# Kernel tuning notes

Hardware: AMD Instinct MI355X
Metric: run time of the kernel (lower is better)

Reference implementation:

```python
import jax, jax.numpy as jnp
import numpy as np

MIN_VAL = 1e-10


def integ_exp_trig(lam, theta, t, t0=None):
    # Analytic integrals of exp(lam*s)*cos(theta*s) and exp(lam*s)*sin(theta*s) on [t0, t].
    if t0 is None:
        t0 = jnp.zeros_like(t)
    exps_t = jnp.nan_to_num(jnp.exp(lam * t))
    exps_t0 = jnp.nan_to_num(jnp.exp(lam * t0))
    denom = jnp.square(lam) + jnp.square(theta)
    scale = jnp.sign(denom) / jnp.clip(denom, MIN_VAL)
    cos_t, sin_t = jnp.cos(theta * t), jnp.sin(theta * t)
    cos_t0, sin_t0 = jnp.cos(theta * t0), jnp.sin(theta * t0)
    res_cos = scale * (exps_t * (lam * cos_t + theta * sin_t)
                       - exps_t0 * (lam * cos_t0 + theta * sin_t0))
    res_sin = scale * (exps_t * (lam * sin_t - theta * cos_t)
                       - exps_t0 * (lam * sin_t0 - theta * cos_t0))
    return jnp.nan_to_num(res_cos), jnp.nan_to_num(res_sin)


def esde_predict_complex(X0, X0_var, U, times, Q, lam_real, lam_imag, V_real, V_imag):
    B, n = X0.shape
    m = n // 2
    lam = lam_real + 1j * lam_imag          # [B, m] complex
    V = V_real + 1j * V_imag                # [B, n, m] complex
    X0c = X0[:, :, None]                    # [B, n, 1]

    # Phi(0): exp(0*lam) = 1, so phi_comp = V
    Phi0 = jnp.concatenate([V.real, V.imag], axis=2)        # [B, n, n]
    Phi0_inv = jnp.nan_to_num(jnp.linalg.inv(Phi0))

    init_cond = Phi0_inv @ X0c                               # [B, n, 1]
    init_var = Phi0_inv @ X0_var @ jnp.swapaxes(Phi0_inv, -1, -2)

    # Phi(t)
    et = jnp.exp(times[:, None].astype(lam.dtype) * lam)     # [B, m] complex
    phi = V * et[:, None, :]                                 # right-mult by diag(et)
    Phi = jnp.nan_to_num(jnp.concatenate([phi.real, phi.imag], axis=2))  # [B, n, n]

    Hom = Phi @ init_cond
    Hom_var = Phi @ init_var @ jnp.swapaxes(Phi, -1, -2)
    # force positive diagonal: diag -> |diag|, off-diag unchanged
    eye = jnp.eye(n, dtype=Hom_var.dtype)
    diag_sign = jnp.sign(jnp.diagonal(Hom_var, axis1=-2, axis2=-1))  # [B, n]
    Hom_var = Hom_var * ((1.0 - eye) + eye * diag_sign[:, :, None])

    # ----- particular (control) term: block 2x2 rotation-integral times Phi0_inv @ U
    ext_u = (Phi0_inv @ U[:, :, None]).reshape(B, m, 2)      # interleaved (re, im) pairs
    cos_int, sin_int = integ_exp_trig(-lam.real, lam.imag, times[:, None])  # [B, m]
    li0 = cos_int * ext_u[..., 0] - sin_int * ext_u[..., 1]
    li1 = sin_int * ext_u[..., 0] + cos_int * ext_u[..., 1]
    lambda_int = jnp.stack([li0, li1], axis=-1).reshape(B, n, 1)
    Part = Phi @ lambda_int

    # ----- diffusion variance term
    ext_s = Phi0_inv @ Q @ jnp.swapaxes(Phi0_inv, -1, -2)    # [B, n, n]
    ls = lam[:, None, :] + lam[:, :, None]                   # lam_i + lam_j
    ls_conj = lam[:, None, :] - lam[:, :, None]              # lam_j - lam_i
    t3 = times[:, None, None]
    cos1, sin1 = integ_exp_trig(-ls.real, ls.imag, t3)       # [B, m, m]
    cos2, sin2 = integ_exp_trig(-ls.real, ls_conj.imag, t3)
    vcc = 0.5 * (cos1 + cos2)   # int cos*cos
    vsc = 0.5 * (sin1 + sin2)   # int sin*cos
    vcs = 0.5 * (sin1 - sin2)   # int cos*sin
    vss = 0.5 * (cos2 - cos1)   # int sin*sin
    E = ext_s.reshape(B, m, 2, m, 2)  # interleaved 2x2 block structure
    d11, d12 = E[:, :, 0, :, 0], E[:, :, 0, :, 1]
    d21, d22 = E[:, :, 1, :, 0], E[:, :, 1, :, 1]
    r11 = vcc * d11 - vsc * d21 - vcs * d12 + vss * d22
    r12 = vcs * d11 - vss * d21 + vcc * d12 - vsc * d22
    r21 = vsc * d11 + vcc * d21 - vss * d12 - vcs * d22
    r22 = vss * d11 + vcs * d21 + vsc * d12 + vcc * d22
    row0 = jnp.stack([r11, r12], axis=-1)   # [B, m, m, 2]
    row1 = jnp.stack([r21, r22], axis=-1)
    sig_int = jnp.stack([row0, row1], axis=2).reshape(B, n, n)
    Part_var = Phi @ sig_int @ jnp.swapaxes(Phi, -1, -2)

    return Hom + Part, Hom_var + Part_var


def setup_inputs() -> dict:
    key = jax.random.key(0)
    ks = jax.random.split(key, 9)
    B, n = 65536, 16
    m = n // 2
    X0 = jax.random.normal(ks[0], (B, n), jnp.float32)
    A = jax.random.normal(ks[1], (B, n, n), jnp.float32) * 0.1
    X0_var = A @ jnp.swapaxes(A, -1, -2) + 0.1 * jnp.eye(n, dtype=jnp.float32)
    U = jax.random.normal(ks[2], (B, n), jnp.float32)
    times = jax.random.uniform(ks[3], (B,), jnp.float32, 0.1, 2.0)
    Qa = jax.random.normal(ks[4], (B, n, n), jnp.float32) * 0.1
    Q = Qa @ jnp.swapaxes(Qa, -1, -2)
    lam_real = -jax.random.uniform(ks[5], (B, m), jnp.float32, 0.05, 1.0)
    lam_imag = jax.random.uniform(ks[6], (B, m), jnp.float32, -2.0, 2.0)
    V_real = jax.random.normal(ks[7], (B, n, m), jnp.float32)
    V_imag = jax.random.normal(ks[8], (B, n, m), jnp.float32)
    return {"X0": X0, "X0_var": X0_var, "U": U, "times": times, "Q": Q,
            "lam_real": lam_real, "lam_imag": lam_imag,
            "V_real": V_real, "V_imag": V_imag}


def reference(X0, X0_var, U, times, Q, lam_real, lam_imag, V_real, V_imag):
    return esde_predict_complex(X0, X0_var, U, times, Q,
                                lam_real, lam_imag, V_real, V_imag)
```

## Files before the change

### kernel.cpp

```cpp
#include <hip/hip_runtime.h>
#include <math.h>

#define WSYNC() do { __builtin_amdgcn_wave_barrier(); asm volatile("" ::: "memory"); } while (0)
#define LFENCE() asm volatile("" ::: "memory")

constexpr int FS = 20;

typedef float v2f __attribute__((ext_vector_type(2)));
__device__ inline v2f pkfma(v2f a, v2f b, v2f c) {
  return __builtin_elementwise_fma(a, b, c);
}

struct alignas(16) WaveMem {
  float P[16 * FS];
  float F[16 * FS];
  float W[16 * FS];
  float L4[16 * FS];
  float etr[8], eti[8], lamr[8], lami[8];
  float vx0[16], vu[16], vic[16];
};

__device__ inline float n2n(float v) {
  if (isnan(v)) return 0.0f;
  if (isinf(v)) return v > 0.f ? 3.402823466e38f : -3.402823466e38f;
  return v;
}

__device__ inline float readlane_f(float v, int l) {
  return __int_as_float(__builtin_amdgcn_readlane(__float_as_int(v), l));
}
template<int CTRL>
__device__ inline float dpp_f(float v) {
  return __int_as_float(__builtin_amdgcn_mov_dpp(__float_as_int(v), CTRL, 0xF, 0xF, true));
}

__device__ inline void load16(float out[16], const float* p) {
#pragma unroll
  for (int c = 0; c < 4; ++c) {
    float4 v = *(const float4*)(p + 4 * c);
    out[4*c+0] = v.x; out[4*c+1] = v.y; out[4*c+2] = v.z; out[4*c+3] = v.w;
  }
}

template<bool TRB>
__device__ inline void mmv(float* C, const float* A, const float* Bm,
                           int i16, int jg, bool absdiag = false)
{
  const int j0 = jg << 2;
  float aA[16];
  load16(aA, &A[i16 * FS]);
  float acc[4];
  if (TRB) {
#pragma unroll
    for (int cp = 0; cp < 2; ++cp) {
      float bB0[16], bB1[16];
      load16(bB0, &Bm[(j0 + 2*cp) * FS]);
      load16(bB1, &Bm[(j0 + 2*cp + 1) * FS]);
      v2f s = {0.f, 0.f};
#pragma unroll
      for (int k = 0; k < 16; ++k)
        s = pkfma((v2f){aA[k], aA[k]}, (v2f){bB0[k], bB1[k]}, s);
      acc[2*cp] = s.x; acc[2*cp+1] = s.y;
    }
  } else {
    v2f a01 = {0.f, 0.f}, a23 = {0.f, 0.f};
#pragma unroll
    for (int k = 0; k < 16; ++k) {
      float4 bv = *(const float4*)&Bm[k * FS + j0];
      v2f ad = {aA[k], aA[k]};
      a01 = pkfma(ad, (v2f){bv.x, bv.y}, a01);
      a23 = pkfma(ad, (v2f){bv.z, bv.w}, a23);
    }
    acc[0] = a01.x; acc[1] = a01.y; acc[2] = a23.x; acc[3] = a23.y;
  }
  if (absdiag) {
#pragma unroll
    for (int c = 0; c < 4; ++c) if (i16 == j0 + c) acc[c] = fabsf(acc[c]);
  }
  *(float4*)&C[i16 * FS + j0] = make_float4(acc[0], acc[1], acc[2], acc[3]);
}

__global__ __launch_bounds__(256, 7) void nesde_kernel(
    const float* __restrict__ gX0, const float* __restrict__ gXv,
    const float* __restrict__ gU,  const float* __restrict__ gT,
    const float* __restrict__ gQ,  const float* __restrict__ gLr,
    const float* __restrict__ gLi, const float* __restrict__ gVr,
    const float* __restrict__ gVi, float* __restrict__ gOut0,
    float* __restrict__ gOut1, int B)
{
  __shared__ WaveMem sm[4];
  const int wid  = threadIdx.x >> 6;
  const int lane = threadIdx.x & 63;
  const int b = blockIdx.x * 4 + wid;
  if (b >= B) return;
  WaveMem& S = sm[wid];

  const int r4  = lane >> 2;
  const int q   = lane & 3;
  const int i16 = lane & 15;
  const int jg  = lane >> 4;
  const int j0  = jg << 2;

  const float t = gT[b];

  const float4 xv = *(const float4*)(gXv + (size_t)b * 256 + lane * 4);
  const float4 qv = *(const float4*)(gQ  + (size_t)b * 256 + lane * 4);
  float4 va = make_float4(0.f,0.f,0.f,0.f), vb = va;
  if (q < 2) {
    const float* src = (q == 0) ? gVr : gVi;
    va = *(const float4*)(src + (size_t)b * 128 + r4 * 8);
    vb = *(const float4*)(src + (size_t)b * 128 + r4 * 8 + 4);
  }
  float x0u = 0.f;
  if (q == 2) x0u = gX0[(size_t)b * 16 + r4];
  if (q == 3) x0u = gU [(size_t)b * 16 + r4];

  if (lane < 8) {
    float lr = gLr[(size_t)b * 8 + lane];
    float li = gLi[(size_t)b * 8 + lane];
    S.lamr[lane] = lr; S.lami[lane] = li;
    float e = expf(lr * t);
    float sn, cs; sincosf(li * t, &sn, &cs);
    S.etr[lane] = e * cs;
    S.eti[lane] = e * sn;
  }
  WSYNC();

  float4 vco;
  {
    const int p = lane >> 3, qq = lane & 7;
    float la  = -(S.lamr[p] + S.lamr[qq]);
    float th1 = S.lami[p] + S.lami[qq];
    float th2 = S.lami[qq] - S.lami[p];
    float exps = __expf(la * t);
    float s1, c1, s2, c2;
    __sincosf(th1 * t, &s1, &c1);
    __sincosf(th2 * t, &s2, &c2);
    float den1 = la * la + th1 * th1;
    float sg1 = (den1 > 0.f) ? 1.f : ((den1 < 0.f) ? -1.f : 0.f);
    float sc1 = sg1 / fmaxf(den1, 1e-10f);
    float cos1 = sc1 * (exps * (la * c1 + th1 * s1) - la);
    float sin1 = sc1 * (exps * (la * s1 - th1 * c1) + th1);
    float den2 = la * la + th2 * th2;
    float sg2 = (den2 > 0.f) ? 1.f : ((den2 < 0.f) ? -1.f : 0.f);
    float sc2 = sg2 / fmaxf(den2, 1e-10f);
    float cos2 = sc2 * (exps * (la * c2 + th2 * s2) - la);
    float sin2 = sc2 * (exps * (la * s2 - th2 * c2) + th2);
    vco = make_float4(0.5f * (cos1 + cos2), 0.5f * (sin1 + sin2),
                      0.5f * (sin1 - sin2), 0.5f * (cos2 - cos1));
  }
  {
    const int si = lane >> 2, sj = (lane & 3) * 4;
    *(float4*)&S.L4[si * FS + sj] = qv;
  }
  if (q == 2) S.vx0[r4] = x0u;
  if (q == 3) S.vu[r4]  = x0u;

  float myv[8] = { va.x, va.y, va.z, va.w, vb.x, vb.y, vb.z, vb.w };
  float ov[8];
#pragma unroll
  for (int e = 0; e < 8; ++e) ov[e] = __shfl_xor(myv[e], 1);
  if (q < 2) {
    float er[8], ei[8];
#pragma unroll
    for (int e = 0; e < 8; ++e) { er[e] = S.etr[e]; ei[e] = S.eti[e]; }
    float vr[8], vi[8], ph[8];
#pragma unroll
    for (int e = 0; e < 8; ++e) {
      vr[e] = (q == 0) ? myv[e] : ov[e];
      vi[e] = (q == 0) ? ov[e]  : myv[e];
    }
    if (q == 0) {
#pragma unroll
      for (int e = 0; e < 8; ++e) ph[e] = vr[e] * er[e] - vi[e] * ei[e];
      *(float4*)&S.F[r4 * FS + 0] = make_float4(ph[0], ph[1], ph[2], ph[3]);
      *(float4*)&S.F[r4 * FS + 4] = make_float4(ph[4], ph[5], ph[6], ph[7]);
    } else {
#pragma unroll
      for (int e = 0; e < 8; ++e) ph[e] = vr[e] * ei[e] + vi[e] * er[e];
      *(float4*)&S.F[r4 * FS + 8]  = make_float4(ph[0], ph[1], ph[2], ph[3]);
      *(float4*)&S.F[r4 * FS + 12] = make_float4(ph[4], ph[5], ph[6], ph[7]);
    }
  }

  float a[8];
#pragma unroll
  for (int e = 0; e < 8; ++e) {
    float idv = 0.f;
    if (q == 2) idv = (r4 == e)     ? 1.f : 0.f;
    if (q == 3) idv = (r4 == 8 + e) ? 1.f : 0.f;
    a[e] = (q < 2) ? myv[e] : idv;
  }

  unsigned used = 0;
  int myk = 0;
#pragma unroll
  for (int k = 0; k < 16; ++k) {
    const int qk = k >> 3, ek = k & 7;
    float av = a[ek];
    float ck = (qk == 0) ? dpp_f<0x00>(av) : dpp_f<0x55>(av);
    float cand = ((used >> r4) & 1u) ? -1.0f : fabsf(ck);
    float mx = cand;
    mx = fmaxf(mx, dpp_f<0x124>(mx));
    mx = fmaxf(mx, dpp_f<0x128>(mx));
    mx = fmaxf(mx, dpp_f<0x142>(mx));
    mx = fmaxf(mx, dpp_f<0x143>(mx));
    float smx = readlane_f(mx, 63);
    unsigned long long msk = __ballot(cand == smx);
    const int pl4 = (__ffsll((long long)msk) - 1) & 60;
    const bool isp = ((lane & 60) == pl4);
    if (isp) {
      *(float4*)&S.W[q * 8]     = make_float4(a[0], a[1], a[2], a[3]);
      *(float4*)&S.W[q * 8 + 4] = make_float4(a[4], a[5], a[6], a[7]);
    }
    float pval = readlane_f(av, pl4 | qk);
    float pivinv = 1.0f / pval;
    LFENCE();
    float4 r0 = *(const float4*)&S.W[q * 8];
    float4 r1 = *(const float4*)&S.W[q * 8 + 4];
    LFENCE();
    float rr[8] = { r0.x, r0.y, r0.z, r0.w, r1.x, r1.y, r1.z, r1.w };
    const v2f pivd = { pivinv, pivinv };
    const v2f nck  = { -ck, -ck };
#pragma unroll
    for (int e2 = 0; e2 < 4; ++e2) {
      v2f rrp = { rr[2*e2], rr[2*e2+1] };
      v2f sp  = rrp * pivd;
      v2f up  = pkfma(nck, sp, (v2f){ a[2*e2], a[2*e2+1] });
      a[2*e2]   = isp ? sp.x : up.x;
      a[2*e2+1] = isp ? sp.y : up.y;
    }
    used |= 1u << (pl4 >> 2);
    if (isp) myk = k;
  }

  if (q >= 2) {
    const int base = myk * FS + ((q - 2) << 3);
    *(float4*)&S.P[base]     = make_float4(n2n(a[0]), n2n(a[1]), n2n(a[2]), n2n(a[3]));
    *(float4*)&S.P[base + 4] = make_float4(n2n(a[4]), n2n(a[5]), n2n(a[6]), n2n(a[7]));
  }
  WSYNC();

  if (lane < 32) {
    const float* src = (lane < 16) ? S.vx0 : S.vu;
    float sv[16], pA[16];
    load16(pA, &S.P[i16 * FS]);
    load16(sv, src);
    float d = 0.f;
#pragma unroll
    for (int k = 0; k < 16; ++k) d = fmaf(pA[k], sv[k], d);
    if (lane < 16) S.vic[i16] = d; else S.vu[i16] = d;
  }
  WSYNC();
  if (lane < 8) {
    float la = -S.lamr[lane], th = S.lami[lane];
    float exps = expf(la * t);
    float sn, cs; sincosf(th * t, &sn, &cs);
    float denom = la * la + th * th;
    float sgn = (denom > 0.f) ? 1.f : ((denom < 0.f) ? -1.f : 0.f);
    float scale = sgn / fmaxf(denom, 1e-10f);
    float ci = scale * (exps * (la * cs + th * sn) - la);
    float si = scale * (exps * (la * sn - th * cs) + th);
    float e0 = S.vu[2 * lane], e1 = S.vu[2 * lane + 1];
    S.vic[2 * lane]     += ci * e0 - si * e1;
    S.vic[2 * lane + 1] += si * e0 + ci * e1;
  }
  WSYNC();
  if (lane < 16) {
    float fA[16], vv[16];
    load16(fA, &S.F[lane * FS]);
    load16(vv, S.vic);
    float d = 0.f;
#pragma unroll
    for (int k = 0; k < 16; ++k) d = fmaf(fA[k], vv[k], d);
    gOut0[(size_t)b * 16 + lane] = d;
  }
  WSYNC();

  mmv<false>(S.L4, S.P, S.L4, i16, jg);        WSYNC();
  mmv<true >(S.L4, S.L4, S.P, i16, jg);        WSYNC();
  {
    mmv<false>(S.P, S.F, S.P, i16, jg);
    const int si = lane >> 2, sj = (lane & 3) * 4;
    *(float4*)&S.W[si * FS + sj] = xv;
  }
  WSYNC();
  mmv<false>(S.W, S.P, S.W, i16, jg);          WSYNC();
  mmv<true >(S.W, S.W, S.P, i16, jg, true);    WSYNC();

  {
    const int p2 = i16 >> 1, aa = i16 & 1;
    const int sA = p2 * 8 + (j0 >> 1);
    float4 c0, c1;
    c0.x = __shfl(vco.x, sA);     c0.y = __shfl(vco.y, sA);
    c0.z = __shfl(vco.z, sA);     c0.w = __shfl(vco.w, sA);
    c1.x = __shfl(vco.x, sA + 1); c1.y = __shfl(vco.y, sA + 1);
    c1.z = __shfl(vco.z, sA + 1); c1.w = __shfl(vco.w, sA + 1);
    float4 top = *(const float4*)&S.L4[(2 * p2) * FS + j0];
    float4 bot = *(const float4*)&S.L4[(2 * p2 + 1) * FS + j0];
    float tl[4] = { top.x, top.y, top.z, top.w };
    float bl[4] = { bot.x, bot.y, bot.z, bot.w };
    float r[4];
#pragma unroll
    for (int uu = 0; uu < 4; ++uu) {
      float4 c = (uu < 2) ? c0 : c1;
      const int off = 2 * (uu >> 1);
      float d11 = tl[off], d12 = tl[off + 1];
      float d21 = bl[off], d22 = bl[off + 1];
      const int bb = uu & 1;
      if (aa == 0)
        r[uu] = (bb == 0) ? (c.x * d11 - c.y * d21 - c.z * d12 + c.w * d22)
                          : (c.z * d11 - c.w * d21 + c.x * d12 - c.y * d22);
      else
        r[uu] = (bb == 0) ? (c.y * d11 + c.x * d21 - c.w * d12 - c.z * d22)
                          : (c.w * d11 + c.z * d21 + c.y * d12 + c.x * d22);
    }
    LFENCE();
    *(float4*)&S.L4[i16 * FS + j0] = make_float4(r[0], r[1], r[2], r[3]);
  }
  WSYNC();
  mmv<false>(S.L4, S.F, S.L4, i16, jg);        WSYNC();

  {
    float aA[16];
    load16(aA, &S.L4[i16 * FS]);
    float acc[4];
#pragma unroll
    for (int cp = 0; cp < 2; ++cp) {
      float bB0[16], bB1[16];
      load16(bB0, &S.F[(j0 + 2*cp) * FS]);
      load16(bB1, &S.F[(j0 + 2*cp + 1) * FS]);
      v2f s = {0.f, 0.f};
#pragma unroll
      for (int k = 0; k < 16; ++k)
        s = pkfma((v2f){aA[k], aA[k]}, (v2f){bB0[k], bB1[k]}, s);
      acc[2*cp] = s.x; acc[2*cp+1] = s.y;
    }
    float4 hv = *(const float4*)&S.W[i16 * FS + j0];
    float4 o = make_float4(hv.x + acc[0], hv.y + acc[1], hv.z + acc[2], hv.w + acc[3]);
    *(float4*)&gOut1[(size_t)b * 256 + i16 * 16 + j0] = o;
  }
}

extern "C" void kernel_launch(void* const* d_in, const int* in_sizes, int n_in,
                              void* d_out, int out_size, void* d_ws, size_t ws_size,
                              hipStream_t stream) {
  const float* X0 = (const float*)d_in[0];
  const float* Xv = (const float*)d_in[1];
  const float* U  = (const float*)d_in[2];
  const float* T  = (const float*)d_in[3];
  const float* Q  = (const float*)d_in[4];
  const float* Lr = (const float*)d_in[5];
  const float* Li = (const float*)d_in[6];
  const float* Vr = (const float*)d_in[7];
  const float* Vi = (const float*)d_in[8];
  const int B = in_sizes[3];
  float* out0 = (float*)d_out;
  float* out1 = (float*)d_out + (size_t)B * 16;
  const int blocks = (B + 3) / 4;
  hipLaunchKernelGGL(nesde_kernel, dim3(blocks), dim3(256), 0, stream,
                     X0, Xv, U, T, Q, Lr, Li, Vr, Vi, out0, out1, B);
}
```

Before: 198.7 us.

## Chain covariance matmuls in registers via quad DPP broadcasts, fewer LDS round-trips

Lanes are remapped so that each group of four lanes owns one row of the 16x16 result. The intermediate product of each chained matmul pair (P·Q·Pᵀ, P·X·Pᵀ, F·L·Fᵀ) is then broadcast within the quad using DPP quad_perm moves, instead of being written to LDS and read back. This removes several LDS stores and loads and several wave barriers, and keeps Hom_var in registers until the final add. In exchange it raises register pressure, so the launch bound drops from 7 to 6 waves per SIMD, which may reduce occupancy.

```diff
diff --git a/kernel.cpp b/kernel.cpp
--- a/kernel.cpp
+++ b/kernel.cpp
@@ -42,45 +42,45 @@
   }
 }
 
-template<bool TRB>
-__device__ inline void mmv(float* C, const float* A, const float* Bm,
-                           int i16, int jg, bool absdiag = false)
-{
-  const int j0 = jg << 2;
-  float aA[16];
-  load16(aA, &A[i16 * FS]);
+__device__ inline void bcast16(float aA[16], float4 acc) {
+  aA[0]  = dpp_f<0x00>(acc.x); aA[1]  = dpp_f<0x00>(acc.y);
+  aA[2]  = dpp_f<0x00>(acc.z); aA[3]  = dpp_f<0x00>(acc.w);
+  aA[4]  = dpp_f<0x55>(acc.x); aA[5]  = dpp_f<0x55>(acc.y);
+  aA[6]  = dpp_f<0x55>(acc.z); aA[7]  = dpp_f<0x55>(acc.w);
+  aA[8]  = dpp_f<0xAA>(acc.x); aA[9]  = dpp_f<0xAA>(acc.y);
+  aA[10] = dpp_f<0xAA>(acc.z); aA[11] = dpp_f<0xAA>(acc.w);
+  aA[12] = dpp_f<0xFF>(acc.x); aA[13] = dpp_f<0xFF>(acc.y);
+  aA[14] = dpp_f<0xFF>(acc.z); aA[15] = dpp_f<0xFF>(acc.w);
+}
+
+__device__ inline float4 dotB(const float aA[16], const float* Bm, int j0, int bs) {
+  v2f a01 = {0.f, 0.f}, a23 = {0.f, 0.f};
+#pragma unroll
+  for (int k = 0; k < 16; ++k) {
+    float4 bv = *(const float4*)&Bm[k * bs + j0];
+    v2f ad = {aA[k], aA[k]};
+    a01 = pkfma(ad, (v2f){bv.x, bv.y}, a01);
+    a23 = pkfma(ad, (v2f){bv.z, bv.w}, a23);
+  }
+  return make_float4(a01.x, a01.y, a23.x, a23.y);
+}
+__device__ inline float4 dotBT(const float aA[16], const float* Bm, int j0) {
   float acc[4];
-  if (TRB) {
-#pragma unroll
-    for (int cp = 0; cp < 2; ++cp) {
-      float bB0[16], bB1[16];
-      load16(bB0, &Bm[(j0 + 2*cp) * FS]);
-      load16(bB1, &Bm[(j0 + 2*cp + 1) * FS]);
-      v2f s = {0.f, 0.f};
-#pragma unroll
-      for (int k = 0; k < 16; ++k)
-        s = pkfma((v2f){aA[k], aA[k]}, (v2f){bB0[k], bB1[k]}, s);
-      acc[2*cp] = s.x; acc[2*cp+1] = s.y;
-    }
-  } else {
-    v2f a01 = {0.f, 0.f}, a23 = {0.f, 0.f};
-#pragma unroll
-    for (int k = 0; k < 16; ++k) {
-      float4 bv = *(const float4*)&Bm[k * FS + j0];
-      v2f ad = {aA[k], aA[k]};
-      a01 = pkfma(ad, (v2f){bv.x, bv.y}, a01);
-      a23 = pkfma(ad, (v2f){bv.z, bv.w}, a23);
-    }
-    acc[0] = a01.x; acc[1] = a01.y; acc[2] = a23.x; acc[3] = a23.y;
-  }
-  if (absdiag) {
-#pragma unroll
-    for (int c = 0; c < 4; ++c) if (i16 == j0 + c) acc[c] = fabsf(acc[c]);
-  }
-  *(float4*)&C[i16 * FS + j0] = make_float4(acc[0], acc[1], acc[2], acc[3]);
-}
-
-__global__ __launch_bounds__(256, 7) void nesde_kernel(
+#pragma unroll
+  for (int cp = 0; cp < 2; ++cp) {
+    float bB0[16], bB1[16];
+    load16(bB0, &Bm[(j0 + 2*cp) * FS]);
+    load16(bB1, &Bm[(j0 + 2*cp + 1) * FS]);
+    v2f s = {0.f, 0.f};
+#pragma unroll
+    for (int k = 0; k < 16; ++k)
+      s = pkfma((v2f){aA[k], aA[k]}, (v2f){bB0[k], bB1[k]}, s);
+    acc[2*cp] = s.x; acc[2*cp+1] = s.y;
+  }
+  return make_float4(acc[0], acc[1], acc[2], acc[3]);
+}
+
+__global__ __launch_bounds__(256, 6) void nesde_kernel(
     const float* __restrict__ gX0, const float* __restrict__ gXv,
     const float* __restrict__ gU,  const float* __restrict__ gT,
     const float* __restrict__ gQ,  const float* __restrict__ gLr,
@@ -98,8 +98,8 @@
   const int r4  = lane >> 2;
   const int q   = lane & 3;
   const int i16 = lane & 15;
-  const int jg  = lane >> 4;
-  const int j0  = jg << 2;
+  const int iR  = lane >> 2;
+  const int j0  = (lane & 3) << 2;
 
   const float t = gT[b];
 
@@ -151,7 +151,8 @@
   }
   {
     const int si = lane >> 2, sj = (lane & 3) * 4;
-    *(float4*)&S.L4[si * FS + sj] = qv;
+    *(float4*)&S.L4[si * FS + sj]   = qv;
+    *(float4*)&S.W[32 + (lane << 2)] = xv;
   }
   if (q == 2) S.vx0[r4] = x0u;
   if (q == 3) S.vu[r4]  = x0u;
@@ -277,19 +278,39 @@
   }
   WSYNC();
 
-  mmv<false>(S.L4, S.P, S.L4, i16, jg);        WSYNC();
-  mmv<true >(S.L4, S.L4, S.P, i16, jg);        WSYNC();
-  {
-    mmv<false>(S.P, S.F, S.P, i16, jg);
-    const int si = lane >> 2, sj = (lane & 3) * 4;
-    *(float4*)&S.W[si * FS + sj] = xv;
-  }
-  WSYNC();
-  mmv<false>(S.W, S.P, S.W, i16, jg);          WSYNC();
-  mmv<true >(S.W, S.W, S.P, i16, jg, true);    WSYNC();
-
-  {
-    const int p2 = i16 >> 1, aa = i16 & 1;
+  float4 we;
+  {
+    float aA[16]; load16(aA, &S.P[iR * FS]);
+    we = dotB(aA, S.L4, j0, FS);
+  }
+  LFENCE();
+  {
+    float aA[16]; bcast16(aA, we);
+    float4 es = dotBT(aA, S.P, j0);
+    *(float4*)&S.L4[iR * FS + j0] = es;
+  }
+  WSYNC();
+  {
+    float aA[16]; load16(aA, &S.F[iR * FS]);
+    float4 m = dotB(aA, S.P, j0, FS);
+    LFENCE();
+    *(float4*)&S.P[iR * FS + j0] = m;
+  }
+  WSYNC();
+  float4 hv;
+  {
+    float aA[16]; load16(aA, &S.P[iR * FS]);
+    float4 t1 = dotB(aA, &S.W[32], j0, 16);
+    float aT[16]; bcast16(aT, t1);
+    hv = dotBT(aT, S.P, j0);
+    if (iR == j0 + 0) hv.x = fabsf(hv.x);
+    if (iR == j0 + 1) hv.y = fabsf(hv.y);
+    if (iR == j0 + 2) hv.z = fabsf(hv.z);
+    if (iR == j0 + 3) hv.w = fabsf(hv.w);
+  }
+  WSYNC();
+  {
+    const int p2 = iR >> 1, aa = iR & 1;
     const int sA = p2 * 8 + (j0 >> 1);
     float4 c0, c1;
     c0.x = __shfl(vco.x, sA);     c0.y = __shfl(vco.y, sA);
@@ -316,29 +337,16 @@
                           : (c.w * d11 + c.z * d21 + c.y * d12 + c.x * d22);
     }
     LFENCE();
-    *(float4*)&S.L4[i16 * FS + j0] = make_float4(r[0], r[1], r[2], r[3]);
-  }
-  WSYNC();
-  mmv<false>(S.L4, S.F, S.L4, i16, jg);        WSYNC();
-
-  {
-    float aA[16];
-    load16(aA, &S.L4[i16 * FS]);
-    float acc[4];
-#pragma unroll
-    for (int cp = 0; cp < 2; ++cp) {
-      float bB0[16], bB1[16];
-      load16(bB0, &S.F[(j0 + 2*cp) * FS]);
-      load16(bB1, &S.F[(j0 + 2*cp + 1) * FS]);
-      v2f s = {0.f, 0.f};
-#pragma unroll
-      for (int k = 0; k < 16; ++k)
-        s = pkfma((v2f){aA[k], aA[k]}, (v2f){bB0[k], bB1[k]}, s);
-      acc[2*cp] = s.x; acc[2*cp+1] = s.y;
-    }
-    float4 hv = *(const float4*)&S.W[i16 * FS + j0];
-    float4 o = make_float4(hv.x + acc[0], hv.y + acc[1], hv.z + acc[2], hv.w + acc[3]);
-    *(float4*)&gOut1[(size_t)b * 256 + i16 * 16 + j0] = o;
+    *(float4*)&S.L4[iR * FS + j0] = make_float4(r[0], r[1], r[2], r[3]);
+  }
+  WSYNC();
+  {
+    float aA[16]; load16(aA, &S.F[iR * FS]);
+    float4 ps = dotB(aA, S.L4, j0, FS);
+    float aP[16]; bcast16(aP, ps);
+    float4 pv = dotBT(aP, S.F, j0);
+    float4 o = make_float4(hv.x + pv.x, hv.y + pv.y, hv.z + pv.z, hv.w + pv.w);
+    *(float4*)&gOut1[(size_t)b * 256 + iR * 16 + j0] = o;
   }
 }
 
```

Result: slower. 298.2 us (+50.1%).
